# Kernel optimization log

Hardware: AMD Instinct MI355X
Metric: run time of the kernel (lower is better)

## Reference

```python
import jax, jax.numpy as jnp
import numpy as np
import math

D_MODEL = 512
HEADS = 8
SHIFT = 1
B, T = 2, 1024


def _layernorm(x, w, b, eps=1e-5):
    mu = jnp.mean(x, -1, keepdims=True)
    var = jnp.mean((x - mu) ** 2, -1, keepdims=True)
    return (x - mu) / jnp.sqrt(var + eps) * w + b


def _l1_cdist(x, w, chunk):
    # x: [N, Din], w: [M, Din] -> [N, M]; chunk over M to bound the broadcast buffer
    N, Din = x.shape
    M = w.shape[0]
    wc = w.reshape(M // chunk, chunk, Din)
    f = lambda wb: jnp.abs(x[:, None, :] - wb[None, :, :]).sum(-1)  # [N, chunk]
    out = jax.lax.map(f, wc)  # [M//chunk, N, chunk]
    return jnp.moveaxis(out, 0, 1).reshape(N, M)


def _proxy_linear(x, w, gain, chunk):
    # ProxyDeltaLinearV68: out = (0.5 - dist_proxy_mean) * gain, dist uses detach trick
    Bx, Tx, Din = x.shape
    xa = jnp.tanh(x).reshape(-1, Din)
    wa = jnp.tanh(w)
    l1 = _l1_cdist(xa, wa, chunk)
    # squared L2 via GEMM (== cdist(p=2)**2), clamped at 0 like torch.cdist
    l2 = jnp.maximum((xa * xa).sum(-1)[:, None] + (wa * wa).sum(-1)[None, :] - 2.0 * (xa @ wa.T), 0.0)
    l1m = l1 / Din
    l2m = l2 / Din
    d = jax.lax.stop_gradient(l1m - l2m) + l2m
    return ((0.5 - d) * gain[None, :]).reshape(Bx, Tx, -1)


def _attention(x, wq_w, wq_g, wk_w, wk_g, wv_w, wv_g, wo_w, wo_b, gamma, rho):
    Bx, Tx, C = x.shape
    H, Dh = HEADS, C // HEADS

    def heads(t):
        return t.reshape(Bx, Tx, H, Dh).transpose(0, 2, 1, 3).reshape(Bx * H, Tx, Dh)

    q = heads(jnp.tanh(_proxy_linear(x, wq_w, wq_g, 32)))
    k = heads(jnp.tanh(_proxy_linear(x, wk_w, wk_g, 32)))
    v = heads(_proxy_linear(x, wv_w, wv_g, 32))
    # pairwise L1 distances, chunked over query positions
    TC = 64
    qr = jnp.moveaxis(q.reshape(Bx * H, Tx // TC, TC, Dh), 1, 0)  # [Tx//TC, BH, TC, Dh]
    f = lambda qb: jnp.abs(qb[:, :, None, :] - k[:, None, :, :]).sum(-1)  # [BH, TC, Tx]
    l1 = jnp.moveaxis(jax.lax.map(f, qr), 0, 1).reshape(Bx * H, Tx, Tx)
    l2 = jnp.maximum((q * q).sum(-1)[:, :, None] + (k * k).sum(-1)[:, None, :]
                     - 2.0 * jnp.einsum('btd,bsd->bts', q, k), 0.0)
    dist = jax.lax.stop_gradient((l1 - l2) / Dh) + l2 / Dh
    dist = dist.reshape(Bx, H, Tx, Tx) * math.sqrt(Dh)
    dsq = dist * dist
    gp = jax.nn.softplus(gamma)[None, :, None, None]
    rp = jax.nn.softplus(rho)[None, :, None, None]
    aw = (1.0 / (1.0 + gp * dsq + 1e-6)) ** rp  # student-t style kernel
    mask = jnp.tril(jnp.ones((Tx, Tx), dtype=bool))
    aw = jnp.where(mask[None, None], aw, 0.0)
    probs = aw / (aw.sum(-1, keepdims=True) + 1e-6)
    out = jnp.einsum('bhts,bhsd->bhtd', probs, v.reshape(Bx, H, Tx, Dh))
    out = out.transpose(0, 2, 1, 3).reshape(Bx, Tx, C)
    return out @ wo_w.T + wo_b


def setup_inputs() -> dict:
    key = jax.random.key(0)
    ks = jax.random.split(key, 10)
    D, Hd = D_MODEL, D_MODEL * 4
    f32 = jnp.float32
    return {
        'x': jax.random.normal(ks[0], (B, T, D), f32),
        'ln1_w': jnp.ones((D,), f32), 'ln1_b': jnp.zeros((D,), f32),
        'wq_w': jax.random.normal(ks[1], (D, D), f32) * 0.1, 'wq_g': jnp.full((D,), 2.0, f32),
        'wk_w': jax.random.normal(ks[2], (D, D), f32) * 0.1, 'wk_g': jnp.full((D,), 2.0, f32),
        'wv_w': jax.random.normal(ks[3], (D, D), f32) * 0.1, 'wv_g': jnp.full((D,), 2.0, f32),
        'wo_w': jax.random.normal(ks[4], (D, D), f32) * 0.02, 'wo_b': jnp.zeros((D,), f32),
        'gamma': jnp.ones((HEADS,), f32), 'rho': jnp.full((HEADS,), 2.0, f32),
        'ln2_w': jnp.ones((D,), f32), 'ln2_b': jnp.zeros((D,), f32),
        'gate_w': jax.random.normal(ks[5], (Hd, D), f32) * 0.1, 'gate_g': jnp.full((Hd,), 2.0, f32),
        'val_w': jax.random.normal(ks[6], (Hd, D), f32) * 0.1, 'val_g': jnp.full((Hd,), 2.0, f32),
        'out_w': jax.random.normal(ks[7], (D, Hd), f32) * 0.1, 'out_g': jnp.full((D,), 2.0, f32),
        'dir_w': jax.random.normal(ks[8], (D,), f32) * 0.1,
    }


def reference(x, ln1_w, ln1_b, wq_w, wq_g, wk_w, wk_g, wv_w, wv_g, wo_w, wo_b,
              gamma, rho, ln2_w, ln2_b, gate_w, gate_g, val_w, val_g, out_w, out_g, dir_w):
    a = _attention(_layernorm(x, ln1_w, ln1_b), wq_w, wq_g, wk_w, wk_g, wv_w, wv_g,
                   wo_w, wo_b, gamma, rho)
    x = x + a  # ATTN_SCALE = 1.0
    h = _layernorm(x, ln2_w, ln2_b)
    gate = jax.nn.silu(_proxy_linear(h, gate_w, gate_g, 32))
    val = _proxy_linear(h, val_w, val_g, 32)
    f = _proxy_linear(gate * val, out_w, out_g, 8)
    # Direction: causal shift of ln2 output, |x_shift - sigmoid(w)|
    xp = jnp.concatenate([jnp.zeros((x.shape[0], SHIFT, x.shape[2]), x.dtype), h[:, :-SHIFT]], axis=1)
    d = jnp.abs(xp - jax.nn.sigmoid(dir_w)[None, None, :])
    return x + f + 0.5 * d  # Delta_SCALE=1.0, DIR_SCALE=0.5, dropout identity (eval)
```

## Files before the change

kernel.cpp:

```cpp
#include <hip/hip_runtime.h>
#include <math.h>


#define NROWS  2048
#define DMODEL 512
#define TSEQ   1024
#define HIDDEN 2048

typedef _Float16 hf;
typedef hf h2 __attribute__((ext_vector_type(2)));
typedef hf h4 __attribute__((ext_vector_type(4)));
typedef hf h8 __attribute__((ext_vector_type(8)));
typedef float f32x4 __attribute__((ext_vector_type(4)));

#if defined(__has_builtin)
#if __has_builtin(__builtin_amdgcn_sad_u8)
#define HAVE_SAD 1
#endif
#if __has_builtin(__builtin_amdgcn_mfma_f32_16x16x32_f16)
#define HAVE_MFMA 1
#endif
#endif

__device__ __forceinline__ unsigned sad8(unsigned a, unsigned b, unsigned c) {
#ifdef HAVE_SAD
  return __builtin_amdgcn_sad_u8(a, b, c);
#else
  unsigned r;
  asm("v_sad_u8 %0, %1, %2, %3" : "=v"(r) : "v"(a), "v"(b), "v"(c));
  return r;
#endif
}

__device__ __forceinline__ float ftanh(float x) {
  const float t = __expf(-2.0f * fabsf(x));
  const float r = (1.0f - t) / (1.0f + t);
  return copysignf(r, x);
}

__device__ __forceinline__ float fpow_ge1(float x, float p) {
  float lg, r;
  asm("v_log_f32 %0, %1" : "=v"(lg) : "v"(x));
  const float e = lg * p;
  asm("v_exp_f32 %0, %1" : "=v"(r) : "v"(e));
  return r;
}

__device__ __forceinline__ unsigned q8(float x) {
  return (unsigned)(int)((x + 1.0f) * 127.5f + 0.5f);
}

struct CP { const float* g0; const float* g1; const float* g2; };

__device__ __forceinline__ void ln_body(
    int n, const float* __restrict__ X, const float* __restrict__ w,
    const float* __restrict__ bb, float* __restrict__ outPlain,
    unsigned char* __restrict__ out8, float4* __restrict__ zf)
{
  const int tid = threadIdx.x;
  if (zf && tid < 130)
    zf[(size_t)n * 130 + tid] = make_float4(0.f, 0.f, 0.f, 0.f);
  const float* row = X + (size_t)n * DMODEL;
  float2 v = *(const float2*)&row[tid * 2];
  float s1 = v.x + v.y;
  float s2 = v.x * v.x + v.y * v.y;
#pragma unroll
  for (int off = 1; off < 64; off <<= 1) {
    s1 += __shfl_xor(s1, off);
    s2 += __shfl_xor(s2, off);
  }
  __shared__ float red[8];
  if ((tid & 63) == 0) { red[(tid >> 6) * 2] = s1; red[(tid >> 6) * 2 + 1] = s2; }
  __syncthreads();
  s1 = red[0] + red[2] + red[4] + red[6];
  s2 = red[1] + red[3] + red[5] + red[7];
  const float mu   = s1 * (1.0f / DMODEL);
  const float var  = s2 * (1.0f / DMODEL) - mu * mu;
  const float rstd = rsqrtf(var + 1e-5f);
  const int d = tid * 2;
  const float y0 = (v.x - mu) * rstd * w[d]     + bb[d];
  const float y1 = (v.y - mu) * rstd * w[d + 1] + bb[d + 1];
  if (outPlain) *(float2*)&outPlain[(size_t)n * DMODEL + d] = make_float2(y0, y1);
  const unsigned a = q8(ftanh(y0)), b = q8(ftanh(y1));
  *(unsigned short*)&out8[(size_t)n * DMODEL + d] = (unsigned short)(a | (b << 8));
}

__device__ __forceinline__ void cvt_body(
    const float* __restrict__ src, unsigned char* __restrict__ dst, int K)
{
  const int t = threadIdx.x & 127;
  for (int k = t * 4; k < K; k += 512) {
    float4 v = *(const float4*)&src[k];
    unsigned pk = q8(ftanh(v.x)) | (q8(ftanh(v.y)) << 8) |
                  (q8(ftanh(v.z)) << 16) | (q8(ftanh(v.w)) << 24);
    *(unsigned*)&dst[k] = pk;
  }
}

__global__ __launch_bounds__(256) void fused1_kernel(
    const float* __restrict__ X, const float* __restrict__ lw,
    const float* __restrict__ lb, unsigned char* __restrict__ x8,
    float4* __restrict__ zf,
    const float* __restrict__ wq, const float* __restrict__ wk,
    const float* __restrict__ wv, unsigned char* __restrict__ w8)
{
  const int b = blockIdx.x;
  if (b < NROWS) { ln_body(b, X, lw, lb, nullptr, x8, zf); return; }
  const int c = b - NROWS;
  const int z = c >> 8, rb = c & 255;
  const float* sb = (z == 0) ? wq : (z == 1) ? wk : wv;
  const int row = rb * 2 + (threadIdx.x >> 7);
  cvt_body(sb + (size_t)row * 512, w8 + ((size_t)z * 512 + row) * 512, 512);
}

__global__ __launch_bounds__(256) void fused6_kernel(
    const float* __restrict__ x2, const float* __restrict__ lw,
    const float* __restrict__ lb, float* __restrict__ hbuf,
    unsigned char* __restrict__ x8,
    const float* __restrict__ gate_w, const float* __restrict__ val_w,
    unsigned char* __restrict__ w8,
    const float* __restrict__ out_w, unsigned char* __restrict__ w9)
{
  const int b = blockIdx.x;
  if (b < NROWS) { ln_body(b, x2, lw, lb, hbuf, x8, nullptr); return; }
  int c = b - NROWS;
  if (c < 2048) {
    const int z = c >> 10, rb = c & 1023;
    const float* sb = z ? val_w : gate_w;
    const int row = rb * 2 + (threadIdx.x >> 7);
    cvt_body(sb + (size_t)row * 512, w8 + ((size_t)z * 2048 + row) * 512, 512);
  } else {
    c -= 2048;
    const int row = c * 2 + (threadIdx.x >> 7);
    cvt_body(out_w + (size_t)row * 2048, w9 + (size_t)row * 2048, 2048);
  }
}

template <int NCD, int EPI>
__global__ __launch_bounds__(256, 8) void cdistq_kernel(
    const unsigned char* __restrict__ X8, const unsigned char* __restrict__ W8,
    CP cp,
    unsigned char* __restrict__ o8a, unsigned char* __restrict__ o8b,
    hf* __restrict__ vt16, unsigned char* __restrict__ gvt8,
    unsigned short* __restrict__ pf,
    int M, int K, int Kc, float invK127)
{
  const int m0 = blockIdx.x * 32, n0 = blockIdx.y * 64;
  const int zc = (EPI == 1) ? blockIdx.z : 0;
  const int kb = (EPI == 3) ? blockIdx.z * Kc : 0;
  constexpr int WROW = NCD * 68 + 4;
  __shared__ __align__(16) unsigned xs[2][16][68];
  __shared__ __align__(16) unsigned ws[2][8][WROW];
  const int tid = threadIdx.x, tx = tid & 15, ty = tid >> 4;
  unsigned acc[NCD][4][2] = {};

  const int rs = tid >> 2, ps = (tid & 3) * 2;
  const int half = tid & 127;
  const int wc = (NCD == 2) ? (tid >> 7) : 0;
  const int wcol = half >> 2, kkw = half & 3;

  const unsigned char* xp = X8 + (size_t)(n0 + rs) * K + kb + (tid & 3) * 8;
  const unsigned char* wq = W8 + (size_t)(zc + wc) * M * K +
                            (size_t)(m0 + wcol) * K + kb + kkw * 8;

  uint2 xv0 = *(const uint2*)xp;
  uint2 xv1 = *(const uint2*)(xp + 32);
  uint2 wv0 = *(const uint2*)wq;
  uint2 wv1 = *(const uint2*)(wq + 32);

  int p = 0;
#pragma unroll 1
  for (int k0 = 0; k0 < Kc; k0 += 64) {
    xs[p][ps + 0][rs] = xv0.x;
    xs[p][ps + 1][rs] = xv0.y;
    xs[p][8 + ps + 0][rs] = xv1.x;
    xs[p][8 + ps + 1][rs] = xv1.y;
    *(uint2*)&ws[p][kkw][wc * 68 + wcol * 2]     = make_uint2(wv0.x, wv0.y);
    *(uint2*)&ws[p][4 + kkw][wc * 68 + wcol * 2] = make_uint2(wv1.x, wv1.y);
    const int kn = (k0 + 64 < Kc) ? k0 + 64 : 0;
    xv0 = *(const uint2*)(xp + kn);
    xv1 = *(const uint2*)(xp + kn + 32);
    wv0 = *(const uint2*)(wq + kn);
    wv1 = *(const uint2*)(wq + kn + 32);
    __syncthreads();

#pragma unroll
    for (int kkp = 0; kkp < 8; kkp++) {
      uint4 a0 = *(const uint4*)&xs[p][kkp * 2 + 0][ty * 4];
      uint4 a1 = *(const uint4*)&xs[p][kkp * 2 + 1][ty * 4];
      const unsigned ae[4] = {a0.x, a0.y, a0.z, a0.w};
      const unsigned ao[4] = {a1.x, a1.y, a1.z, a1.w};
#pragma unroll
      for (int c = 0; c < NCD; c++) {
        uint4 b4 = *(const uint4*)&ws[p][kkp][c * 68 + tx * 4];
#pragma unroll
        for (int i = 0; i < 4; i++) {
          acc[c][i][0] = sad8(ae[i], b4.x, acc[c][i][0]);
          acc[c][i][0] = sad8(ao[i], b4.y, acc[c][i][0]);
          acc[c][i][1] = sad8(ae[i], b4.z, acc[c][i][1]);
          acc[c][i][1] = sad8(ao[i], b4.w, acc[c][i][1]);
        }
      }
    }
    p ^= 1;
  }

  if constexpr (EPI == 1) {
    if (zc < 2) {
      unsigned char* o8 = zc ? o8b : o8a;
      const float* gn = zc ? cp.g1 : cp.g0;
#pragma unroll
      for (int i = 0; i < 4; i++) {
        const int n = n0 + ty * 4 + i;
        unsigned pk = 0;
#pragma unroll
        for (int j = 0; j < 2; j++) {
          const int m = m0 + tx * 2 + j;
          const float val = (0.5f - (float)acc[0][i][j] * invK127) * gn[m];
          pk |= q8(ftanh(val)) << (8 * j);
        }
        *(unsigned short*)&o8[(size_t)n * M + m0 + tx * 2] = (unsigned short)pk;
      }
    } else {
#pragma unroll
      for (int i = 0; i < 4; i++) {
        const int n = n0 + ty * 4 + i;
        const int b = n >> 10, t = n & 1023;
#pragma unroll
        for (int j = 0; j < 2; j++) {
          const int m = m0 + tx * 2 + j;
          const float vv = (0.5f - (float)acc[0][i][j] * invK127) * cp.g2[m];
          vt16[((size_t)(b * 8 + (m >> 6)) * 64 + (m & 63)) * 1024 + t] = (hf)vv;
        }
      }
    }
  } else if constexpr (EPI == 2) {
#pragma unroll
    for (int i = 0; i < 4; i++) {
      const int n = n0 + ty * 4 + i;
      unsigned pk = 0;
#pragma unroll
      for (int j = 0; j < 2; j++) {
        const int m = m0 + tx * 2 + j;
        float g = (0.5f - (float)acc[0][i][j] * invK127) * cp.g0[m];
        g = g / (1.0f + __expf(-g));
        const float vv = (0.5f - (float)acc[1][i][j] * invK127) * cp.g1[m];
        pk |= q8(ftanh(g * vv)) << (8 * j);
      }
      *(unsigned short*)&gvt8[(size_t)n * M + m0 + tx * 2] = (unsigned short)pk;
    }
  } else {
    unsigned short* pz = pf + (size_t)blockIdx.z * ((size_t)NROWS * M);
#pragma unroll
    for (int i = 0; i < 4; i++) {
      const int n = n0 + ty * 4 + i;
      const unsigned p0 = (acc[0][i][0] + 1) >> 1;
      const unsigned p1 = (acc[0][i][1] + 1) >> 1;
      *(unsigned*)&pz[(size_t)n * M + m0 + tx * 2] = p0 | (p1 << 16);
    }
  }
}

__global__ __launch_bounds__(256) void attn_part_kernel(
    const unsigned char* __restrict__ Qb, const unsigned char* __restrict__ Kb,
    const hf* __restrict__ Vt,
    const float* __restrict__ gamma, const float* __restrict__ rho,
    float* __restrict__ accO, float* __restrict__ accR)
{
  const int bh = blockIdx.y, b = bh >> 3, h = bh & 7;
  int rem = 143 - (int)blockIdx.x;
  int tt = 0;
  for (;;) {
    const int nc = ((tt >> 1) + 2) >> 1;
    if (rem < nc) break;
    rem -= nc; ++tt;
  }
  const int ntile = (tt >> 1) + 1;
  const int sb = rem * 2;
  const int se = (sb + 2 < ntile) ? sb + 2 : ntile;
  const int t0 = tt * 32;

  const float gp = log1pf(expf(gamma[h]));
  const float nrp = -log1pf(expf(rho[h]));
  const size_t base8 = ((size_t)b * TSEQ) * DMODEL + h * 64;

  __shared__ unsigned qs8[16][36];
  __shared__ unsigned ks8[16][68];
  __shared__ hf awt[32][72];
  __shared__ hf vsm[64][72];

  const int tid = threadIdx.x, tx = tid & 15, ty = tid >> 4;
  const int tx4 = tx * 4, ty2 = ty * 2;
  const int lane = tid & 63, wv = tid >> 6;
  const float SCALE_D = 1.0f / (127.5f * 8.0f);

  {
    const int r = tid >> 3, p = (tid & 7) * 2;
    uint2 a = *(const uint2*)&Qb[base8 + (size_t)(t0 + r) * DMODEL + (tid & 7) * 8];
    qs8[p + 0][r] = a.x;
    qs8[p + 1][r] = a.y;
  }

  float rsum[2] = {};
  f32x4 cacc[2] = {};

  const int vd = tid >> 2, vs16 = (tid & 3) * 16;
  const int arow = lane & 15;
  const int koff = (lane >> 4) * 8;

  for (int st = sb; st < se; ++st) {
    const int s0 = st * 64;
    __syncthreads();
    {
      const int r = tid >> 2, p = (tid & 3) * 4;
      uint4 a = *(const uint4*)&Kb[base8 + (size_t)(s0 + r) * DMODEL + (tid & 3) * 16];
      ks8[p + 0][r] = a.x;
      ks8[p + 1][r] = a.y;
      ks8[p + 2][r] = a.z;
      ks8[p + 3][r] = a.w;
      const hf* vsrc = &Vt[((size_t)bh * 64 + vd) * 1024 + s0 + vs16];
      *(h8*)&vsm[vd][vs16 + 0] = *(const h8*)vsrc;
      *(h8*)&vsm[vd][vs16 + 8] = *(const h8*)(vsrc + 8);
    }
    __syncthreads();

    unsigned sacc[2][4] = {};
#pragma unroll
    for (int kk = 0; kk < 16; kk++) {
      uint2 qa = *(const uint2*)&qs8[kk][ty2];
      uint4 kb4 = *(const uint4*)&ks8[kk][tx4];
      const unsigned kk4[4] = {kb4.x, kb4.y, kb4.z, kb4.w};
#pragma unroll
      for (int j = 0; j < 4; j++) {
        sacc[0][j] = sad8(qa.x, kk4[j], sacc[0][j]);
        sacc[1][j] = sad8(qa.y, kk4[j], sacc[1][j]);
      }
    }

#pragma unroll
    for (int i = 0; i < 2; i++) {
      const int tg = t0 + ty2 + i;
      h4 pk;
#pragma unroll
      for (int j = 0; j < 4; j++) {
        const int sg = s0 + tx4 + j;
        const float dist = (float)sacc[i][j] * SCALE_D;
        const float bsx = fmaf(gp, dist * dist, 1.0f + 1e-6f);
        float aw = fpow_ge1(bsx, nrp);
        aw = (sg <= tg) ? aw : 0.0f;
        pk[j] = (hf)aw;
        rsum[i] += aw;
      }
      *(h4*)&awt[ty2 + i][tx4] = pk;
    }
    __syncthreads();

#ifdef HAVE_MFMA
#pragma unroll
    for (int ks = 0; ks < 2; ks++) {
      h8 bfrag = *(const h8*)&vsm[wv * 16 + arow][ks * 32 + koff];
      h8 afr0  = *(const h8*)&awt[arow]          [ks * 32 + koff];
      h8 afr1  = *(const h8*)&awt[16 + arow]     [ks * 32 + koff];
      cacc[0] = __builtin_amdgcn_mfma_f32_16x16x32_f16(afr0, bfrag, cacc[0], 0, 0, 0);
      cacc[1] = __builtin_amdgcn_mfma_f32_16x16x32_f16(afr1, bfrag, cacc[1], 0, 0, 0);
    }
#else
    {
      const int crow = (lane >> 4) * 4;
      const int d = wv * 16 + (lane & 15);
#pragma unroll
      for (int mt = 0; mt < 2; mt++)
#pragma unroll
        for (int r = 0; r < 4; r++) {
          const int t = mt * 16 + crow + r;
          float s = cacc[mt][r];
          for (int si = 0; si < 64; si++)
            s += (float)awt[t][si] * (float)vsm[d][si];
          cacc[mt][r] = s;
        }
    }
#endif
  }

#pragma unroll
  for (int off = 1; off < 16; off <<= 1) {
    rsum[0] += __shfl_xor(rsum[0], off);
    rsum[1] += __shfl_xor(rsum[1], off);
  }
  float* aO = accO + ((size_t)bh * TSEQ + t0) * 64;
  {
    const int crow = (lane >> 4) * 4;
    const int ccol = wv * 16 + (lane & 15);
#pragma unroll
    for (int mt = 0; mt < 2; mt++)
#pragma unroll
      for (int r = 0; r < 4; r++)
        atomicAdd(&aO[(size_t)(mt * 16 + crow + r) * 64 + ccol], cacc[mt][r]);
  }
#pragma unroll
  for (int i = 0; i < 2; i++)
    if (tx == 0) atomicAdd(&accR[bh * TSEQ + t0 + ty2 + i], rsum[i]);
}

__global__ __launch_bounds__(256) void gemm_res_kernel(
    const float* __restrict__ Xn, const float* __restrict__ accR,
    const float* __restrict__ W,
    const float* __restrict__ bias, const float* __restrict__ Res,
    float* __restrict__ Out)
{
  const int m0 = blockIdx.x * 64, n0 = blockIdx.y * 64;
  __shared__ float xs[16][68];
  __shared__ float wsm[16][68];
  const int tid = threadIdx.x, tx = tid & 15, ty = tid >> 4;
  const int lr = tid >> 2, lc4 = (tid & 3) * 4;
  float acc[4][4] = {};
  const int n = n0 + lr;
  const float* wp = &W[(size_t)(m0 + lr) * DMODEL + lc4];
  for (int k0 = 0; k0 < DMODEL; k0 += 16) {
    const int c = k0 + lc4;
    const size_t arow = ((size_t)((n >> 10) * 8 + (c >> 6))) * TSEQ + (n & 1023);
    float4 xv = *(const float4*)&Xn[arow * 64 + (c & 63)];
    const float inv = 1.0f / (accR[arow] + 1e-6f);
    xv.x *= inv; xv.y *= inv; xv.z *= inv; xv.w *= inv;
    float4 wv = *(const float4*)(wp + k0);
    __syncthreads();
    xs [lc4 + 0][lr] = xv.x; xs [lc4 + 1][lr] = xv.y; xs [lc4 + 2][lr] = xv.z; xs [lc4 + 3][lr] = xv.w;
    wsm[lc4 + 0][lr] = wv.x; wsm[lc4 + 1][lr] = wv.y; wsm[lc4 + 2][lr] = wv.z; wsm[lc4 + 3][lr] = wv.w;
    __syncthreads();
#pragma unroll
    for (int kk = 0; kk < 16; kk++) {
      float4 av = *(const float4*)&xs[kk][ty * 4];
      float4 bv = *(const float4*)&wsm[kk][tx * 4];
      const float aa[4] = {av.x, av.y, av.z, av.w};
      const float bs[4] = {bv.x, bv.y, bv.z, bv.w};
#pragma unroll
      for (int i = 0; i < 4; i++)
#pragma unroll
        for (int j = 0; j < 4; j++) acc[i][j] = fmaf(aa[i], bs[j], acc[i][j]);
    }
  }
#pragma unroll
  for (int i = 0; i < 4; i++) {
    const int nn = n0 + ty * 4 + i;
    float o[4];
#pragma unroll
    for (int j = 0; j < 4; j++) {
      const int m = m0 + tx * 4 + j;
      o[j] = acc[i][j] + bias[m] + Res[(size_t)nn * DMODEL + m];
    }
    *(float4*)&Out[(size_t)nn * DMODEL + m0 + tx * 4] = make_float4(o[0], o[1], o[2], o[3]);
  }
}

__global__ void final_kernel(const float* __restrict__ x2,
                             const unsigned short* __restrict__ pf,
                             const float* __restrict__ outg,
                             const float* __restrict__ h,
                             const float* __restrict__ dirw,
                             float* __restrict__ out)
{
  const int i4 = blockIdx.x * 256 + threadIdx.x;
  const int n = i4 >> 7;
  const int t = n & (TSEQ - 1);
  const int d4 = (i4 & 127) * 4;
  float4 xv = *(const float4*)&x2[(size_t)i4 * 4];
  const size_t off = (size_t)i4 * 4;
  unsigned s[4] = {};
#pragma unroll
  for (int z = 0; z < 4; z++) {
    uint2 a = *(const uint2*)&pf[(size_t)z * ((size_t)NROWS * DMODEL) + off];
    s[0] += (a.x & 0xffffu);
    s[1] += (a.x >> 16);
    s[2] += (a.y & 0xffffu);
    s[3] += (a.y >> 16);
  }
  float4 hv = make_float4(0.f, 0.f, 0.f, 0.f);
  if (t != 0) hv = *(const float4*)&h[(size_t)(i4 - 128) * 4];
  const float xx[4] = {xv.x, xv.y, xv.z, xv.w};
  const float hh[4] = {hv.x, hv.y, hv.z, hv.w};
  const float invf = 2.0f / (127.5f * 2048.0f);
  float o[4];
#pragma unroll
  for (int j = 0; j < 4; j++) {
    const float f = (0.5f - (float)s[j] * invf) * outg[d4 + j];
    const float sg = 1.0f / (1.0f + __expf(-dirw[d4 + j]));
    o[j] = xx[j] + f + 0.5f * fabsf(hh[j] - sg);
  }
  *(float4*)&out[(size_t)i4 * 4] = make_float4(o[0], o[1], o[2], o[3]);
}

extern "C" void kernel_launch(void* const* d_in, const int* in_sizes, int n_in,
                              void* d_out, int out_size, void* d_ws, size_t ws_size,
                              hipStream_t stream)
{
  (void)in_sizes; (void)n_in; (void)out_size;
  const float* x      = (const float*)d_in[0];
  const float* ln1_w  = (const float*)d_in[1];
  const float* ln1_b  = (const float*)d_in[2];
  const float* wq_w   = (const float*)d_in[3];
  const float* wq_g   = (const float*)d_in[4];
  const float* wk_w   = (const float*)d_in[5];
  const float* wk_g   = (const float*)d_in[6];
  const float* wv_w   = (const float*)d_in[7];
  const float* wv_g   = (const float*)d_in[8];
  const float* wo_w   = (const float*)d_in[9];
  const float* wo_b   = (const float*)d_in[10];
  const float* gamma  = (const float*)d_in[11];
  const float* rho    = (const float*)d_in[12];
  const float* ln2_w  = (const float*)d_in[13];
  const float* ln2_b  = (const float*)d_in[14];
  const float* gate_w = (const float*)d_in[15];
  const float* gate_g = (const float*)d_in[16];
  const float* val_w  = (const float*)d_in[17];
  const float* val_g  = (const float*)d_in[18];
  const float* out_w  = (const float*)d_in[19];
  const float* out_g  = (const float*)d_in[20];
  const float* dir_w  = (const float*)d_in[21];
  float* out = (float*)d_out;

  if (ws_size < ((size_t)32 << 20)) return;
  unsigned char* wsb = (unsigned char*)d_ws;

  unsigned char* w8   = wsb;
  unsigned char* x8   = wsb + ((size_t)2 << 20);
  unsigned char* q8b  = wsb + ((size_t)3 << 20);
  unsigned char* k8b  = wsb + ((size_t)4 << 20);
  hf*            vt16 = (hf*)(wsb + ((size_t)5 << 20));
  unsigned char* w9   = wsb + ((size_t)5 << 20);
  unsigned char* gvt8 = wsb + ((size_t)7 << 20);
  float*         accO = (float*)(wsb + ((size_t)11 << 20));
  float*         accR = (float*)(wsb + ((size_t)15 << 20));
  unsigned short* pf  = (unsigned short*)(wsb + ((size_t)16 << 20));
  float*         x2   = (float*)(wsb + ((size_t)24 << 20));
  float*         hbuf = (float*)(wsb + ((size_t)28 << 20));

  fused1_kernel<<<NROWS + 768, 256, 0, stream>>>(
      x, ln1_w, ln1_b, x8, (float4*)accO, wq_w, wk_w, wv_w, w8);

  {
    CP cp; cp.g0 = wq_g; cp.g1 = wk_g; cp.g2 = wv_g;
    cdistq_kernel<1, 1><<<dim3(16, 32, 3), 256, 0, stream>>>(
        x8, w8, cp, q8b, k8b, vt16, nullptr, nullptr,
        512, 512, 512, 1.0f / (127.5f * 512.0f));
  }

  attn_part_kernel<<<dim3(144, 16), 256, 0, stream>>>(q8b, k8b, vt16,
                                                      gamma, rho, accO, accR);

  gemm_res_kernel<<<dim3(8, 32), 256, 0, stream>>>(accO, accR, wo_w, wo_b, x, x2);

  fused6_kernel<<<NROWS + 2048 + 256, 256, 0, stream>>>(
      x2, ln2_w, ln2_b, hbuf, x8, gate_w, val_w, w8, out_w, w9);

  {
    CP cp; cp.g0 = gate_g; cp.g1 = val_g; cp.g2 = nullptr;
    cdistq_kernel<2, 2><<<dim3(64, 32, 1), 256, 0, stream>>>(
        x8, w8, cp, nullptr, nullptr, nullptr, gvt8, nullptr,
        2048, 512, 512, 1.0f / (127.5f * 512.0f));
  }

  {
    CP cp; cp.g0 = out_g; cp.g1 = nullptr; cp.g2 = nullptr;
    cdistq_kernel<1, 3><<<dim3(16, 32, 4), 256, 0, stream>>>(
        gvt8, w9, cp, nullptr, nullptr, nullptr, nullptr, pf,
        512, 2048, 512, 0.0f);
  }

  final_kernel<<<1024, 256, 0, stream>>>(x2, pf, out_g, hbuf, dir_w, out);
}
```

Measured before the change: 150.8 us.

## Port output projection GEMM to fp16 MFMA and raise wave priority in hot loops

The output-projection GEMM with residual is rewritten to convert the normalized attention output and weights to fp16 in shared memory and use 16x16x32 MFMA instructions. Its tile shrinks to 32 rows, which doubles the grid. Separately, s_setprio is raised around the SAD inner loop of the cdist kernel and the MFMA section of the attention kernel so compute phases get issue priority over loading waves. The fp16 conversion lowers the precision of the projection inputs, and the new epilogue writes scalar values instead of float4.

```diff
diff --git a/kernel.cpp b/kernel.cpp
--- a/kernel.cpp
+++ b/kernel.cpp
@@ -184,6 +184,7 @@
     wv1 = *(const uint2*)(wq + kn + 32);
     __syncthreads();
 
+    __builtin_amdgcn_s_setprio(1);
 #pragma unroll
     for (int kkp = 0; kkp < 8; kkp++) {
       uint4 a0 = *(const uint4*)&xs[p][kkp * 2 + 0][ty * 4];
@@ -202,6 +203,7 @@
         }
       }
     }
+    __builtin_amdgcn_s_setprio(0);
     p ^= 1;
   }
 
@@ -356,6 +358,7 @@
     __syncthreads();
 
 #ifdef HAVE_MFMA
+    __builtin_amdgcn_s_setprio(1);
 #pragma unroll
     for (int ks = 0; ks < 2; ks++) {
       h8 bfrag = *(const h8*)&vsm[wv * 16 + arow][ks * 32 + koff];
@@ -364,6 +367,7 @@
       cacc[0] = __builtin_amdgcn_mfma_f32_16x16x32_f16(afr0, bfrag, cacc[0], 0, 0, 0);
       cacc[1] = __builtin_amdgcn_mfma_f32_16x16x32_f16(afr1, bfrag, cacc[1], 0, 0, 0);
     }
+    __builtin_amdgcn_s_setprio(0);
 #else
     {
       const int crow = (lane >> 4) * 4;
@@ -408,48 +412,65 @@
     const float* __restrict__ bias, const float* __restrict__ Res,
     float* __restrict__ Out)
 {
-  const int m0 = blockIdx.x * 64, n0 = blockIdx.y * 64;
-  __shared__ float xs[16][68];
-  __shared__ float wsm[16][68];
-  const int tid = threadIdx.x, tx = tid & 15, ty = tid >> 4;
-  const int lr = tid >> 2, lc4 = (tid & 3) * 4;
-  float acc[4][4] = {};
-  const int n = n0 + lr;
-  const float* wp = &W[(size_t)(m0 + lr) * DMODEL + lc4];
-  for (int k0 = 0; k0 < DMODEL; k0 += 16) {
-    const int c = k0 + lc4;
-    const size_t arow = ((size_t)((n >> 10) * 8 + (c >> 6))) * TSEQ + (n & 1023);
-    float4 xv = *(const float4*)&Xn[arow * 64 + (c & 63)];
-    const float inv = 1.0f / (accR[arow] + 1e-6f);
-    xv.x *= inv; xv.y *= inv; xv.z *= inv; xv.w *= inv;
-    float4 wv = *(const float4*)(wp + k0);
+  const int m0 = blockIdx.x * 64, n0 = blockIdx.y * 32;
+  __shared__ hf xnb[32][40];
+  __shared__ hf wb[64][40];
+  const int tid = threadIdx.x, lane = tid & 63, wv = tid >> 6;
+  const int arow = lane & 15, koff = (lane >> 4) * 8;
+  f32x4 acc0 = {}, acc1 = {};
+  const int xr = tid >> 3, xk = (tid & 7) * 4;
+  const int wr = tid >> 2, wk = (tid & 3) * 8;
+  const int n = n0 + xr;
+
+  for (int k0 = 0; k0 < DMODEL; k0 += 32) {
+    const int c = k0 + xk;
+    const size_t ar = ((size_t)((n >> 10) * 8 + (c >> 6))) * TSEQ + (n & 1023);
+    float4 xv = *(const float4*)&Xn[ar * 64 + (c & 63)];
+    const float inv = 1.0f / (accR[ar] + 1e-6f);
+    float4 w0 = *(const float4*)&W[(size_t)(m0 + wr) * DMODEL + k0 + wk];
+    float4 w1 = *(const float4*)&W[(size_t)(m0 + wr) * DMODEL + k0 + wk + 4];
     __syncthreads();
-    xs [lc4 + 0][lr] = xv.x; xs [lc4 + 1][lr] = xv.y; xs [lc4 + 2][lr] = xv.z; xs [lc4 + 3][lr] = xv.w;
-    wsm[lc4 + 0][lr] = wv.x; wsm[lc4 + 1][lr] = wv.y; wsm[lc4 + 2][lr] = wv.z; wsm[lc4 + 3][lr] = wv.w;
+    h4 xh = { (hf)(xv.x * inv), (hf)(xv.y * inv),
+              (hf)(xv.z * inv), (hf)(xv.w * inv) };
+    *(h4*)&xnb[xr][xk] = xh;
+    h8 wh = { (hf)w0.x, (hf)w0.y, (hf)w0.z, (hf)w0.w,
+              (hf)w1.x, (hf)w1.y, (hf)w1.z, (hf)w1.w };
+    *(h8*)&wb[wr][wk] = wh;
     __syncthreads();
-#pragma unroll
-    for (int kk = 0; kk < 16; kk++) {
-      float4 av = *(const float4*)&xs[kk][ty * 4];
-      float4 bv = *(const float4*)&wsm[kk][tx * 4];
-      const float aa[4] = {av.x, av.y, av.z, av.w};
-      const float bs[4] = {bv.x, bv.y, bv.z, bv.w};
-#pragma unroll
-      for (int i = 0; i < 4; i++)
-#pragma unroll
-        for (int j = 0; j < 4; j++) acc[i][j] = fmaf(aa[i], bs[j], acc[i][j]);
-    }
-  }
-#pragma unroll
-  for (int i = 0; i < 4; i++) {
-    const int nn = n0 + ty * 4 + i;
-    float o[4];
-#pragma unroll
-    for (int j = 0; j < 4; j++) {
-      const int m = m0 + tx * 4 + j;
-      o[j] = acc[i][j] + bias[m] + Res[(size_t)nn * DMODEL + m];
-    }
-    *(float4*)&Out[(size_t)nn * DMODEL + m0 + tx * 4] = make_float4(o[0], o[1], o[2], o[3]);
-  }
+#ifdef HAVE_MFMA
+    h8 bfrag = *(const h8*)&wb[wv * 16 + arow][koff];
+    h8 a0 = *(const h8*)&xnb[arow][koff];
+    h8 a1 = *(const h8*)&xnb[16 + arow][koff];
+    acc0 = __builtin_amdgcn_mfma_f32_16x16x32_f16(a0, bfrag, acc0, 0, 0, 0);
+    acc1 = __builtin_amdgcn_mfma_f32_16x16x32_f16(a1, bfrag, acc1, 0, 0, 0);
+#else
+    {
+      const int crow = (lane >> 4) * 4;
+      const int m = wv * 16 + (lane & 15);
+#pragma unroll
+      for (int s = 0; s < 2; s++)
+#pragma unroll
+        for (int r = 0; r < 4; r++) {
+          float sacc = s ? acc1[r] : acc0[r];
+          const int nn = s * 16 + crow + r;
+          for (int kk = 0; kk < 32; kk++)
+            sacc += (float)xnb[nn][kk] * (float)wb[m][kk];
+          if (s) acc1[r] = sacc; else acc0[r] = sacc;
+        }
+    }
+#endif
+  }
+  const int crow = (lane >> 4) * 4;
+  const int ccol = m0 + wv * 16 + (lane & 15);
+  const float bv = bias[ccol];
+#pragma unroll
+  for (int s = 0; s < 2; s++)
+#pragma unroll
+    for (int r = 0; r < 4; r++) {
+      const int nn = n0 + s * 16 + crow + r;
+      const float v = s ? acc1[r] : acc0[r];
+      Out[(size_t)nn * DMODEL + ccol] = v + bv + Res[(size_t)nn * DMODEL + ccol];
+    }
 }
 
 __global__ void final_kernel(const float* __restrict__ x2,
@@ -547,7 +568,7 @@
   attn_part_kernel<<<dim3(144, 16), 256, 0, stream>>>(q8b, k8b, vt16,
                                                       gamma, rho, accO, accR);
 
-  gemm_res_kernel<<<dim3(8, 32), 256, 0, stream>>>(accO, accR, wo_w, wo_b, x, x2);
+  gemm_res_kernel<<<dim3(8, 64), 256, 0, stream>>>(accO, accR, wo_w, wo_b, x, x2);
 
   fused6_kernel<<<NROWS + 2048 + 256, 256, 0, stream>>>(
       x2, ln2_w, ln2_b, hbuf, x8, gate_w, val_w, w8, out_w, w9);
```

After: 132.6 us. -12.1%, faster.
